# Kernel tuning notes

Hardware: AMD Instinct MI355X
Metric: run time of the kernel (lower is better)

Reference implementation:

```python
import jax, jax.numpy as jnp
import numpy as np

B, T, C = 4, 2048, 1024
HEADS = 16
HEAD_DIM = C // HEADS
WINDOW = 256


def setup_inputs() -> dict:
    key = jax.random.key(0)
    k1, k2, k3 = jax.random.split(key, 3)
    x = jax.random.normal(k1, (B, T, C), dtype=jnp.float32)
    # torch nn.Linear weights: [out_features, in_features]; scale like kaiming-uniform-ish
    W_qkv = jax.random.normal(k2, (3 * C, C), dtype=jnp.float32) * (1.0 / np.sqrt(C))
    W_proj = jax.random.normal(k3, (C, C), dtype=jnp.float32) * (1.0 / np.sqrt(C))
    return {"x": x, "W_qkv": W_qkv, "W_proj": W_proj}


def reference(x, W_qkv, W_proj):
    b, t, c = x.shape
    h, d = HEADS, HEAD_DIM
    qkv = x @ W_qkv.T  # [b,t,3c]
    q, k, v = jnp.split(qkv, 3, axis=-1)
    q = q.reshape(b, t, h, d).transpose(0, 2, 1, 3)  # [b,h,t,d]
    k = k.reshape(b, t, h, d).transpose(0, 2, 1, 3)
    v = v.reshape(b, t, h, d).transpose(0, 2, 1, 3)
    scale = 1.0 / jnp.sqrt(jnp.asarray(d, dtype=q.dtype))
    scores = jnp.einsum('bhqd,bhkd->bhqk', q, k) * scale  # [b,h,t,t]
    i = jnp.arange(t)[:, None]
    j = jnp.arange(t)[None, :]
    mask = (j <= i) & (j > i - WINDOW)  # sliding-window causal band
    scores = jnp.where(mask, scores, -jnp.inf)
    attn = jax.nn.softmax(scores, axis=-1)
    y = jnp.einsum('bhqk,bhkd->bhqd', attn, v)  # [b,h,t,d]
    y = y.transpose(0, 2, 1, 3).reshape(b, t, c)
    return y @ W_proj.T
```

## Files before the change

kernel.cpp:

```cpp
#include <hip/hip_runtime.h>
#include <hip/hip_bf16.h>
#include <math.h>

#define BB 4
#define TT 2048
#define CC 1024
#define HH 16
#define DD 64
#define WW 256
#define MM (BB*TT)
#define NX (MM*CC)
#define NQ (3*CC*CC)
#define NP (CC*CC)

typedef __bf16 bf16x8 __attribute__((ext_vector_type(8)));
typedef __bf16 bf16x4 __attribute__((ext_vector_type(4)));
typedef float  f32x4  __attribute__((ext_vector_type(4)));

__device__ __forceinline__ void async_cp16(const void* g, void* l) {
  __builtin_amdgcn_global_load_lds(
      (const __attribute__((address_space(1))) void*)g,
      (__attribute__((address_space(3))) void*)l, 16, 0, 0);
}

__device__ __forceinline__ unsigned short f2bf(float v) {
  __hip_bfloat16 h = __float2bfloat16(v);
  return *(unsigned short*)&h;
}

__global__ __launch_bounds__(256)
void prep(const float* __restrict__ x,
          const float* __restrict__ wq,
          const float* __restrict__ wp,
          __hip_bfloat16* __restrict__ wdst,
          unsigned short* __restrict__ Apk) {
  const int p = blockIdx.x;
  const int tid = threadIdx.x;
  if (p < 4096) {
    int i = (p * 256 + tid) * 4;
    const float* src; int off;
    if (i < NQ) { src = wq; off = i; }
    else        { src = wp; off = i - NQ; }
    float4 v = *(const float4*)(src + off);
    wdst[i + 0] = __float2bfloat16(v.x);
    wdst[i + 1] = __float2bfloat16(v.y);
    wdst[i + 2] = __float2bfloat16(v.z);
    wdst[i + 3] = __float2bfloat16(v.w);
    return;
  }
  __shared__ __align__(16) unsigned short tile[64 * 72];
  const int pid = p - 4096;
  const int bm = pid & 127;
  const int bk = pid >> 7;
  const int tr = tid >> 4;
  const int tc = (tid & 15) * 4;
#pragma unroll
  for (int i = 0; i < 4; i++) {
    int row = i * 16 + tr;
    float4 v = *(const float4*)&x[(size_t)(bm * 64 + row) * 1024 + bk * 64 + tc];
    tile[row * 72 + tc + 0] = f2bf(v.x);
    tile[row * 72 + tc + 1] = f2bf(v.y);
    tile[row * 72 + tc + 2] = f2bf(v.z);
    tile[row * 72 + tc + 3] = f2bf(v.w);
  }
  __syncthreads();
  const int w = tid >> 6, lane = tid & 63;
  const int quad = lane >> 4, l15 = lane & 15;
#pragma unroll
  for (int f = 0; f < 2; f++) {
    bf16x8 fr = *(const bf16x8*)&tile[(w * 16 + l15) * 72 + f * 32 + quad * 8];
    *(bf16x8*)&Apk[(((size_t)(bm * 4 + w) * 32) + bk * 2 + f) * 512 + lane * 8] = fr;
  }
}

__global__ __launch_bounds__(256, 2)
void gemm_qkv(const unsigned short* __restrict__ Apk,
              const unsigned short* __restrict__ Bw,
              unsigned short* __restrict__ Qh,
              unsigned short* __restrict__ Kh,
              unsigned short* __restrict__ Vt) {
  __shared__ __align__(16) unsigned short Bs0[16 * 1024];
  __shared__ __align__(16) unsigned short Bs1[16 * 1024];

  const int id   = blockIdx.x;
  const int xcd  = id & 7;
  const int slot = id >> 3;
  const int mloc = slot / 24;
  const int nloc = slot % 24;
  const int m0 = (xcd * 4 + mloc) * 256;
  const int n0 = nloc * 128;

  const int tid  = threadIdx.x;
  const int w    = tid >> 6;
  const int lane = tid & 63;
  const int quad = lane >> 4;
  const int l15  = lane & 15;

  f32x4 acc[4][8];
#pragma unroll
  for (int i = 0; i < 4; i++)
#pragma unroll
    for (int j = 0; j < 8; j++) acc[i][j] = (f32x4)0.0f;

  const unsigned short* abase =
      Apk + ((size_t)((m0 >> 4) + w * 4) * 32) * 512 + lane * 8;

  auto stageB = [&](int k0, unsigned short* bs) {
#pragma unroll
    for (int i = 0; i < 8; i++) {
      int idx  = w + 4 * i;
      int kc   = idx >> 1;
      int half = idx & 1;
      async_cp16(Bw + (size_t)(n0 + half * 64 + lane) * 1024 + k0 + kc * 8,
                 &bs[kc * 1024 + half * 512]);
    }
  };

  bf16x8 Af[3][4];
  auto loadA = [&](int g, bf16x8* fr) {
#pragma unroll
    for (int tm = 0; tm < 4; tm++)
      fr[tm] = *(const bf16x8*)(abase + ((size_t)(tm * 32 + g)) * 512);
  };

  loadA(0, Af[0]);
  loadA(1, Af[1]);
  stageB(0, Bs0);
  __syncthreads();

#pragma unroll
  for (int s = 0; s < 8; s++) {
    const unsigned short* bs = (s & 1) ? Bs1 : Bs0;
    if (s + 1 < 8) stageB((s + 1) * 128, (s & 1) ? Bs0 : Bs1);
#pragma unroll
    for (int sub = 0; sub < 4; sub++) {
      const int g = s * 4 + sub;
      if (g + 2 < 32) loadA(g + 2, Af[(g + 2) % 3]);
      const bf16x8* af = Af[g % 3];
#pragma unroll
      for (int tn = 0; tn < 8; tn++) {
        bf16x8 bfv = *(const bf16x8*)
            &bs[(sub * 4 + quad) * 1024 + (tn * 16 + l15) * 8];
#pragma unroll
        for (int tm = 0; tm < 4; tm++)
          acc[tm][tn] = __builtin_amdgcn_mfma_f32_16x16x32_bf16(
              af[tm], bfv, acc[tm][tn], 0, 0, 0);
      }
    }
    __syncthreads();
  }

  const int t3 = n0 >> 10;
  if (t3 < 2) {
    unsigned short* dst0 = (t3 == 0) ? Qh : Kh;
    const float sc = (t3 == 0) ? 0.125f : 1.0f;
#pragma unroll
    for (int tm = 0; tm < 4; tm++)
#pragma unroll
      for (int tn = 0; tn < 8; tn++) {
        int colb = n0 + tn * 16;
        int hh = (colb >> 6) & 15;
        int dd = (colb & 63) + l15;
#pragma unroll
        for (int r = 0; r < 4; r++) {
          int row = m0 + w * 64 + tm * 16 + quad * 4 + r;
          int b = row >> 11, tt = row & 2047;
          dst0[((size_t)((b * 16 + hh) * 2048 + tt)) * 64 + dd] =
              f2bf(acc[tm][tn][r] * sc);
        }
      }
  } else {
    unsigned short* T = (w < 3) ? (Bs0 + w * 4608) : Bs1;
    const int b    = (m0 + w * 64) >> 11;
    const int tc_g = ((m0 & 2047) >> 6) + w;
    const int h0   = (n0 >> 6) & 15;
#pragma unroll
    for (int hp = 0; hp < 2; hp++) {
#pragma unroll
      for (int tnl = 0; tnl < 4; tnl++)
#pragma unroll
        for (int tm = 0; tm < 4; tm++)
#pragma unroll
          for (int r = 0; r < 4; r++)
            T[(tnl * 16 + l15) * 72 + tm * 16 + quad * 4 + r] =
                f2bf(acc[tm][hp * 4 + tnl][r]);
      asm volatile("s_waitcnt lgkmcnt(0)" ::: "memory");
      const size_t base =
          ((size_t)((b * 16 + h0 + hp) * 32 + tc_g)) * 4096;
#pragma unroll
      for (int i = 0; i < 8; i++) {
        int d   = i * 8 + (lane >> 3);
        int tin = (lane & 7) * 8;
        bf16x8 v = *(const bf16x8*)&T[d * 72 + tin];
        *(bf16x8*)&Vt[base + (size_t)d * 64 + tin] = v;
      }
    }
  }
}

__global__ __launch_bounds__(256, 2)
void gemm_proj(const unsigned short* __restrict__ Apk,
               const unsigned short* __restrict__ Bw,
               float* __restrict__ Co) {
  __shared__ __align__(16) unsigned short Bs0[16 * 1024];
  __shared__ __align__(16) unsigned short Bs1[16 * 1024];

  const int id   = blockIdx.x;
  const int xcd  = id & 7;
  const int slot = id >> 3;
  const int mloc = slot >> 3;
  const int nloc = slot & 7;
  const int m0 = (xcd * 8 + mloc) * 128;
  const int n0 = nloc * 128;

  const int tid  = threadIdx.x;
  const int w    = tid >> 6;
  const int lane = tid & 63;
  const int quad = lane >> 4;
  const int l15  = lane & 15;

  f32x4 acc[2][8];
#pragma unroll
  for (int i = 0; i < 2; i++)
#pragma unroll
    for (int j = 0; j < 8; j++) acc[i][j] = (f32x4)0.0f;

  const unsigned short* abase =
      Apk + ((size_t)((m0 >> 4) + w * 2) * 32) * 512 + lane * 8;

  auto stageB = [&](int k0, unsigned short* bs) {
#pragma unroll
    for (int i = 0; i < 8; i++) {
      int idx  = w + 4 * i;
      int kc   = idx >> 1;
      int half = idx & 1;
      async_cp16(Bw + (size_t)(n0 + half * 64 + lane) * 1024 + k0 + kc * 8,
                 &bs[kc * 1024 + half * 512]);
    }
  };

  bf16x8 Af[3][2];
  auto loadA = [&](int g, bf16x8* fr) {
#pragma unroll
    for (int tm = 0; tm < 2; tm++)
      fr[tm] = *(const bf16x8*)(abase + ((size_t)(tm * 32 + g)) * 512);
  };

  loadA(0, Af[0]);
  loadA(1, Af[1]);
  stageB(0, Bs0);
  __syncthreads();

#pragma unroll
  for (int s = 0; s < 8; s++) {
    const unsigned short* bs = (s & 1) ? Bs1 : Bs0;
    if (s + 1 < 8) stageB((s + 1) * 128, (s & 1) ? Bs0 : Bs1);
#pragma unroll
    for (int sub = 0; sub < 4; sub++) {
      const int g = s * 4 + sub;
      if (g + 2 < 32) loadA(g + 2, Af[(g + 2) % 3]);
      const bf16x8* af = Af[g % 3];
#pragma unroll
      for (int tn = 0; tn < 8; tn++) {
        bf16x8 bfv = *(const bf16x8*)
            &bs[(sub * 4 + quad) * 1024 + (tn * 16 + l15) * 8];
#pragma unroll
        for (int tm = 0; tm < 2; tm++)
          acc[tm][tn] = __builtin_amdgcn_mfma_f32_16x16x32_bf16(
              af[tm], bfv, acc[tm][tn], 0, 0, 0);
      }
    }
    __syncthreads();
  }

#pragma unroll
  for (int tm = 0; tm < 2; tm++)
#pragma unroll
    for (int tn = 0; tn < 8; tn++)
#pragma unroll
      for (int r = 0; r < 4; r++) {
        int row = m0 + w * 32 + tm * 16 + quad * 4 + r;
        int col = n0 + tn * 16 + l15;
        Co[(size_t)row * 1024 + col] = acc[tm][tn][r];
      }
}

__global__ __launch_bounds__(256, 2)
void attn_mfma(const unsigned short* __restrict__ Qh,
               const unsigned short* __restrict__ Kh,
               const unsigned short* __restrict__ Vt,
               unsigned short* __restrict__ Ypk) {
  __shared__ __align__(16) unsigned short SH[40960];

  const int tid  = threadIdx.x;
  const int w    = tid >> 6;
  const int lane = tid & 63;
  const int quad = lane >> 4;
  const int l15  = lane & 15;
  const int q0 = blockIdx.x * 64;
  const int bh = blockIdx.y;

  const int c0 = (q0 >= 256) ? 0 : (4 - (q0 >> 6));

  const unsigned short* Qg = Qh + ((size_t)bh * 2048 + q0) * 64;
  bf16x8 Qf[2];
#pragma unroll
  for (int fs = 0; fs < 2; fs++)
    Qf[fs] = *(const bf16x8*)(Qg + (w * 16 + l15) * 64 + fs * 32 + quad * 8);

  const unsigned short* Kg = Kh + (size_t)bh * 2048 * 64;
  const unsigned short* Vg = Vt + (size_t)bh * 32 * 4096;
  for (int ch = c0; ch < 5; ch++) {
    int sc = q0 - 256 + ch * 64;
#pragma unroll
    for (int i = 0; i < 2; i++) {
      int kc = w * 2 + i;
      async_cp16(Kg + (size_t)(sc + lane) * 64 + kc * 8,
                 &SH[ch * 4096 + kc * 512]);
      async_cp16(Vg + (size_t)(sc >> 6) * 4096 + lane * 64 + kc * 8,
                 &SH[20480 + ch * 4096 + kc * 512]);
    }
  }
  __syncthreads();

  f32x4 S[5][4];
#pragma unroll
  for (int ch = 0; ch < 5; ch++)
#pragma unroll
    for (int tn = 0; tn < 4; tn++) S[ch][tn] = (f32x4)0.0f;

#pragma unroll
  for (int ch = 0; ch < 5; ch++) {
    if (ch < c0) continue;
#pragma unroll
    for (int ks = 0; ks < 2; ks++) {
      int kc = ks * 4 + quad;
#pragma unroll
      for (int tn = 0; tn < 4; tn++) {
        bf16x8 bk = *(const bf16x8*)
            &SH[ch * 4096 + kc * 512 + (tn * 16 + l15) * 8];
        S[ch][tn] = __builtin_amdgcn_mfma_f32_16x16x32_bf16(
            Qf[ks], bk, S[ch][tn], 0, 0, 0);
      }
    }
  }

  const int qb = q0 + w * 16 + quad * 4;
  if (c0 == 0) {
#pragma unroll
    for (int tn = 0; tn < 4; tn++) {
      int j = q0 - 256 + tn * 16 + l15;
#pragma unroll
      for (int r = 0; r < 4; r++)
        if (qb + r > j + (WW - 1)) S[0][tn][r] = -__builtin_inff();
    }
  }
#pragma unroll
  for (int tn = 0; tn < 4; tn++) {
    int j = q0 + tn * 16 + l15;
#pragma unroll
    for (int r = 0; r < 4; r++)
      if (j > qb + r) S[4][tn][r] = -__builtin_inff();
  }

  float mrow[4], lrow[4];
#pragma unroll
  for (int r = 0; r < 4; r++) mrow[r] = -__builtin_inff();
#pragma unroll
  for (int ch = 0; ch < 5; ch++) {
    if (ch < c0) continue;
#pragma unroll
    for (int tn = 0; tn < 4; tn++)
#pragma unroll
      for (int r = 0; r < 4; r++)
        mrow[r] = fmaxf(mrow[r], S[ch][tn][r]);
  }
#pragma unroll
  for (int off = 1; off < 16; off <<= 1)
#pragma unroll
    for (int r = 0; r < 4; r++)
      mrow[r] = fmaxf(mrow[r], __shfl_xor(mrow[r], off));

#pragma unroll
  for (int r = 0; r < 4; r++) lrow[r] = 0.0f;
#pragma unroll
  for (int ch = 0; ch < 5; ch++) {
    if (ch < c0) continue;
#pragma unroll
    for (int tn = 0; tn < 4; tn++)
#pragma unroll
      for (int r = 0; r < 4; r++) {
        float e = __expf(S[ch][tn][r] - mrow[r]);
        S[ch][tn][r] = e;
        lrow[r] += e;
      }
  }
#pragma unroll
  for (int off = 1; off < 16; off <<= 1)
#pragma unroll
    for (int r = 0; r < 4; r++) lrow[r] += __shfl_xor(lrow[r], off);

  __syncthreads();

  f32x4 Oacc[4];
#pragma unroll
  for (int td = 0; td < 4; td++) Oacc[td] = (f32x4)0.0f;

#pragma unroll
  for (int ch = 0; ch < 5; ch++) {
    if (ch < c0) continue;
    unsigned short* Ps = SH + (ch & 1) * 4608;
#pragma unroll
    for (int tn = 0; tn < 4; tn++)
#pragma unroll
      for (int r = 0; r < 4; r++)
        Ps[(w * 16 + quad * 4 + r) * 68 + tn * 16 + l15] = f2bf(S[ch][tn][r]);
    asm volatile("s_waitcnt lgkmcnt(0)" ::: "memory");
#pragma unroll
    for (int ks = 0; ks < 2; ks++) {
      int off = (w * 16 + l15) * 68 + ks * 32 + quad * 8;
      bf16x4 plo = *(const bf16x4*)&Ps[off];
      bf16x4 phi = *(const bf16x4*)&Ps[off + 4];
      bf16x8 ap = __builtin_shufflevector(plo, phi, 0, 1, 2, 3, 4, 5, 6, 7);
      int kc = ks * 4 + quad;
#pragma unroll
      for (int td = 0; td < 4; td++) {
        bf16x8 bv = *(const bf16x8*)
            &SH[20480 + ch * 4096 + kc * 512 + (td * 16 + l15) * 8];
        Oacc[td] = __builtin_amdgcn_mfma_f32_16x16x32_bf16(
            ap, bv, Oacc[td], 0, 0, 0);
      }
    }
  }

  const int b = bh >> 4, h = bh & 15;
  float inv[4];
#pragma unroll
  for (int r = 0; r < 4; r++) inv[r] = 1.0f / lrow[r];
  unsigned short* Ot = SH + 10240;
#pragma unroll
  for (int td = 0; td < 4; td++)
#pragma unroll
    for (int r = 0; r < 4; r++)
      Ot[(w * 16 + quad * 4 + r) * 72 + td * 16 + l15] =
          f2bf(Oacc[td][r] * inv[r]);
  asm volatile("s_waitcnt lgkmcnt(0)" ::: "memory");
  const size_t rt = (size_t)((b * 2048 + q0) >> 4) + w;
#pragma unroll
  for (int f = 0; f < 2; f++) {
    bf16x8 fr = *(const bf16x8*)&Ot[(w * 16 + l15) * 72 + f * 32 + quad * 8];
    *(bf16x8*)&Ypk[(rt * 32 + h * 2 + f) * 512 + lane * 8] = fr;
  }
}

extern "C" void kernel_launch(void* const* d_in, const int* in_sizes, int n_in,
                              void* d_out, int out_size, void* d_ws, size_t ws_size,
                              hipStream_t stream) {
  const float* x     = (const float*)d_in[0];
  const float* wqkv  = (const float*)d_in[1];
  const float* wproj = (const float*)d_in[2];
  float* out = (float*)d_out;

  char* ws = (char*)d_ws;
  unsigned short* apk    = (unsigned short*)(ws);
  unsigned short* wqkvb  = (unsigned short*)(ws + (size_t)16 * 1024 * 1024);
  unsigned short* wprojb = (unsigned short*)(ws + (size_t)22 * 1024 * 1024);
  unsigned short* qh     = (unsigned short*)(ws + (size_t)24 * 1024 * 1024);
  unsigned short* kh     = (unsigned short*)(ws + (size_t)40 * 1024 * 1024);
  unsigned short* vt     = (unsigned short*)(ws + (size_t)56 * 1024 * 1024);
  unsigned short* ypk    = (unsigned short*)(ws + (size_t)72 * 1024 * 1024);

  prep<<<4096 + 2048, 256, 0, stream>>>(
      x, wqkv, wproj, (__hip_bfloat16*)wqkvb, apk);

  gemm_qkv<<<768, 256, 0, stream>>>(apk, wqkvb, qh, kh, vt);

  attn_mfma<<<dim3(TT / 64, BB * HH), 256, 0, stream>>>(
      qh, kh, vt, ypk);

  gemm_proj<<<512, 256, 0, stream>>>(ypk, wprojb, out);
}
```

Before: 225.7 us.

## Deepen GEMM B-tile pipeline to four 64-K buffers with fine-grained waits

Both the QKV and projection GEMMs now stage the weight tile in four 64-wide K buffers, prefetched three stages ahead, instead of two 128-wide buffers. The full __syncthreads is replaced by explicit s_waitcnt vmcnt/lgkmcnt counts plus a raw s_barrier, so only the next buffer's async loads have to land before each stage. MFMA sections are also raised in priority with s_setprio. The goal is to hide global-to-LDS latency better at the same LDS footprint, in exchange for twice as many barriers and hand-tuned vmcnt values that depend on the exact load count and are easy to get wrong.

```diff
diff --git a/kernel.cpp b/kernel.cpp
--- a/kernel.cpp
+++ b/kernel.cpp
@@ -79,8 +79,7 @@
               unsigned short* __restrict__ Qh,
               unsigned short* __restrict__ Kh,
               unsigned short* __restrict__ Vt) {
-  __shared__ __align__(16) unsigned short Bs0[16 * 1024];
-  __shared__ __align__(16) unsigned short Bs1[16 * 1024];
+  __shared__ __align__(16) unsigned short Bs[4][8192];
 
   const int id   = blockIdx.x;
   const int xcd  = id & 7;
@@ -107,7 +106,7 @@
 
   auto stageB = [&](int k0, unsigned short* bs) {
 #pragma unroll
-    for (int i = 0; i < 8; i++) {
+    for (int i = 0; i < 4; i++) {
       int idx  = w + 4 * i;
       int kc   = idx >> 1;
       int half = idx & 1;
@@ -125,18 +124,23 @@
 
   loadA(0, Af[0]);
   loadA(1, Af[1]);
-  stageB(0, Bs0);
-  __syncthreads();
-
-#pragma unroll
-  for (int s = 0; s < 8; s++) {
-    const unsigned short* bs = (s & 1) ? Bs1 : Bs0;
-    if (s + 1 < 8) stageB((s + 1) * 128, (s & 1) ? Bs0 : Bs1);
-#pragma unroll
-    for (int sub = 0; sub < 4; sub++) {
-      const int g = s * 4 + sub;
+  stageB(0,   Bs[0]);
+  stageB(64,  Bs[1]);
+  stageB(128, Bs[2]);
+  asm volatile("s_waitcnt vmcnt(0)" ::: "memory");
+  __builtin_amdgcn_sched_barrier(0);
+  asm volatile("s_barrier" ::: "memory");
+
+#pragma unroll
+  for (int s = 0; s < 16; s++) {
+    const unsigned short* bs = Bs[s & 3];
+    if (s + 3 < 16) stageB((s + 3) * 64, Bs[(s + 3) & 3]);
+#pragma unroll
+    for (int sub = 0; sub < 2; sub++) {
+      const int g = s * 2 + sub;
       if (g + 2 < 32) loadA(g + 2, Af[(g + 2) % 3]);
       const bf16x8* af = Af[g % 3];
+      __builtin_amdgcn_s_setprio(1);
 #pragma unroll
       for (int tn = 0; tn < 8; tn++) {
         bf16x8 bfv = *(const bf16x8*)
@@ -146,8 +150,11 @@
           acc[tm][tn] = __builtin_amdgcn_mfma_f32_16x16x32_bf16(
               af[tm], bfv, acc[tm][tn], 0, 0, 0);
       }
-    }
-    __syncthreads();
+      __builtin_amdgcn_s_setprio(0);
+    }
+    asm volatile("s_waitcnt vmcnt(16) lgkmcnt(0)" ::: "memory");
+    __builtin_amdgcn_sched_barrier(0);
+    asm volatile("s_barrier" ::: "memory");
   }
 
   const int t3 = n0 >> 10;
@@ -170,7 +177,7 @@
         }
       }
   } else {
-    unsigned short* T = (w < 3) ? (Bs0 + w * 4608) : Bs1;
+    unsigned short* T = &Bs[0][0] + w * 4608;
     const int b    = (m0 + w * 64) >> 11;
     const int tc_g = ((m0 & 2047) >> 6) + w;
     const int h0   = (n0 >> 6) & 15;
@@ -202,8 +209,7 @@
 void gemm_proj(const unsigned short* __restrict__ Apk,
                const unsigned short* __restrict__ Bw,
                float* __restrict__ Co) {
-  __shared__ __align__(16) unsigned short Bs0[16 * 1024];
-  __shared__ __align__(16) unsigned short Bs1[16 * 1024];
+  __shared__ __align__(16) unsigned short Bs[4][8192];
 
   const int id   = blockIdx.x;
   const int xcd  = id & 7;
@@ -230,7 +236,7 @@
 
   auto stageB = [&](int k0, unsigned short* bs) {
 #pragma unroll
-    for (int i = 0; i < 8; i++) {
+    for (int i = 0; i < 4; i++) {
       int idx  = w + 4 * i;
       int kc   = idx >> 1;
       int half = idx & 1;
@@ -248,18 +254,23 @@
 
   loadA(0, Af[0]);
   loadA(1, Af[1]);
-  stageB(0, Bs0);
-  __syncthreads();
-
-#pragma unroll
-  for (int s = 0; s < 8; s++) {
-    const unsigned short* bs = (s & 1) ? Bs1 : Bs0;
-    if (s + 1 < 8) stageB((s + 1) * 128, (s & 1) ? Bs0 : Bs1);
-#pragma unroll
-    for (int sub = 0; sub < 4; sub++) {
-      const int g = s * 4 + sub;
+  stageB(0,   Bs[0]);
+  stageB(64,  Bs[1]);
+  stageB(128, Bs[2]);
+  asm volatile("s_waitcnt vmcnt(0)" ::: "memory");
+  __builtin_amdgcn_sched_barrier(0);
+  asm volatile("s_barrier" ::: "memory");
+
+#pragma unroll
+  for (int s = 0; s < 16; s++) {
+    const unsigned short* bs = Bs[s & 3];
+    if (s + 3 < 16) stageB((s + 3) * 64, Bs[(s + 3) & 3]);
+#pragma unroll
+    for (int sub = 0; sub < 2; sub++) {
+      const int g = s * 2 + sub;
       if (g + 2 < 32) loadA(g + 2, Af[(g + 2) % 3]);
       const bf16x8* af = Af[g % 3];
+      __builtin_amdgcn_s_setprio(1);
 #pragma unroll
       for (int tn = 0; tn < 8; tn++) {
         bf16x8 bfv = *(const bf16x8*)
@@ -269,8 +280,14 @@
           acc[tm][tn] = __builtin_amdgcn_mfma_f32_16x16x32_bf16(
               af[tm], bfv, acc[tm][tn], 0, 0, 0);
       }
-    }
-    __syncthreads();
+      __builtin_amdgcn_s_setprio(0);
+    }
+    if (s < 14)
+      asm volatile("s_waitcnt vmcnt(12) lgkmcnt(0)" ::: "memory");
+    else
+      asm volatile("s_waitcnt vmcnt(8) lgkmcnt(0)" ::: "memory");
+    __builtin_amdgcn_sched_barrier(0);
+    asm volatile("s_barrier" ::: "memory");
   }
 
 #pragma unroll
```

New measurement: 219.2 us. -2.9%, faster.
